# Kernel optimization log

Measured on AMD Instinct MI355X. Metric: run time of the kernel, lower is better.

The kernel has to match this reference:

```python
import jax, jax.numpy as jnp
import numpy as np

OUT = 260        # RESIZE_OUTPUT_IMAGES_SHAPE
TH = 0.8         # OD_SCORE_TH
PCT = 1.0        # INTERNAL_PERCENTAGE_IMAGE_TOTAKE
N_BOXES = 10     # loop bound in original call()
TAPS = 6         # lanczos3 support (radius 3 -> 6 taps, antialias=False)


def _lanczos_taps(src, size):
    """src: (OUT,) float sample coords in crop-local space; size: traced int crop size.
    Returns clamped tap indices (OUT,6) and normalized lanczos3 weights (OUT,6)."""
    base = jnp.floor(src).astype(jnp.int32) - 2
    taps = base[:, None] + jnp.arange(TAPS, dtype=jnp.int32)          # (OUT,6)
    d = src[:, None] - taps.astype(src.dtype)
    w = jnp.where(jnp.abs(d) < 3.0, jnp.sinc(d) * jnp.sinc(d / 3.0), 0.0)
    w = w / jnp.sum(w, axis=1, keepdims=True)
    idx = jnp.clip(taps, 0, size - 1)
    return idx, w


def _crop_resize(img, box):
    """img: (H,W,3). box: (4,) normalized [ymin,xmin,ymax,xmax] -> (OUT,OUT,3).
    Matches tf.image.resize lanczos3 (antialias=False): half-pixel centers, clamped edges."""
    H, W = img.shape[0], img.shape[1]
    y0 = (box[0] * H).astype(jnp.int32)
    x0 = (box[1] * W).astype(jnp.int32)
    y1 = (box[2] * H).astype(jnp.int32)
    x1 = (box[3] * W).astype(jnp.int32)
    ch = jnp.maximum(y1 - y0, 1)
    cw = jnp.maximum(x1 - x0, 1)
    o = jnp.arange(OUT, dtype=img.dtype)
    src_h = (o + 0.5) * (ch.astype(img.dtype) / OUT) - 0.5
    src_w = (o + 0.5) * (cw.astype(img.dtype) / OUT) - 0.5
    idx_h, w_h = _lanczos_taps(src_h, ch)
    idx_w, w_w = _lanczos_taps(src_w, cw)
    idx_h = idx_h + y0
    idx_w = idx_w + x0
    # vertical pass: gather 6 row taps per output row, reduce -> (OUT, W, 3)
    rows = jnp.einsum('pa,pawc->pwc', w_h, img[idx_h])
    # horizontal pass: gather 6 col taps per output col, reduce -> (OUT, OUT, 3)
    out = jnp.einsum('qb,pqbc->pqc', w_w, rows[:, idx_w])
    return out


def setup_inputs() -> dict:
    key = jax.random.key(0)
    k1, k2, k3, k4 = jax.random.split(key, 4)
    # scores: first 10 mostly above threshold, rest below
    s_hi = 0.85 + 0.15 * jax.random.uniform(k1, (N_BOXES,), dtype=jnp.float32)
    s_lo = 0.8 * jax.random.uniform(k2, (100 - N_BOXES,), dtype=jnp.float32)
    od_scores = jnp.concatenate([s_hi, s_lo])
    # bboxes (ymin,xmin,ymax,xmax) with guaranteed positive crop sizes
    u = jax.random.uniform(k3, (100, 4), dtype=jnp.float32)
    od_bboxes = jnp.stack([u[:, 0] * 0.45, u[:, 1] * 0.45,
                           0.55 + 0.45 * u[:, 2], 0.55 + 0.45 * u[:, 3]], axis=1)
    image = jax.random.normal(k4, (1, 2048, 2048, 3), dtype=jnp.float32)
    return {"od_scores": od_scores, "od_bboxes": od_bboxes, "image": image}


def reference(od_scores, od_bboxes, image):
    img = image[0]                           # (H,W,3)
    b10 = od_bboxes[:N_BOXES]
    s10 = od_scores[:N_BOXES]
    valid = ((od_scores[0] >= TH) & (s10 >= TH)
             & (b10[:, 1] >= 0.5 - PCT / 2.0)
             & (b10[:, 3] <= 0.5 + PCT / 2.0))
    crops = jax.vmap(lambda b: _crop_resize(img, b))(b10)   # (10,OUT,OUT,3)
    return crops * valid[:, None, None, None].astype(img.dtype)
```

## Files before the change

### kernel.cpp

```cpp
#include <hip/hip_runtime.h>
#include <math.h>

#define OUT 260
#define IMG_H 2048
#define IMG_W 2048
#define NB 10
#define TH 0.8f

__device__ __forceinline__ float sincf(float x) {
    if (x == 0.0f) return 1.0f;
    float px = 3.14159265358979323846f * x;
    return __sinf(px) / px;
}

__global__ __launch_bounds__(256) void crop_resize_kernel(
    const float* __restrict__ scores,
    const float* __restrict__ boxes,
    const float* __restrict__ img,
    float* __restrict__ out)
{
    const int p   = blockIdx.x;
    const int box = blockIdx.y;

    const float b0 = boxes[box * 4 + 0];
    const float b1 = boxes[box * 4 + 1];
    const float b2 = boxes[box * 4 + 2];
    const float b3 = boxes[box * 4 + 3];

    const int y0 = (int)(b0 * (float)IMG_H);
    const int x0 = (int)(b1 * (float)IMG_W);
    const int y1 = (int)(b2 * (float)IMG_H);
    const int x1 = (int)(b3 * (float)IMG_W);
    const int ch = max(y1 - y0, 1);
    const int cw = max(x1 - x0, 1);

    const bool valid = (scores[0] >= TH) && (scores[box] >= TH)
                    && (b1 >= 0.0f) && (b3 <= 1.0f);
    const float vmask = valid ? 1.0f : 0.0f;

    float wh[6];
    int   ih[6];
    {
        const float src = ((float)p + 0.5f) * ((float)ch / (float)OUT) - 0.5f;
        const int base = (int)floorf(src) - 2;
        float s = 0.0f;
        #pragma unroll
        for (int a = 0; a < 6; ++a) {
            const int tap = base + a;
            const float d = src - (float)tap;
            const float w = (fabsf(d) < 3.0f) ? sincf(d) * sincf(d * (1.0f / 3.0f)) : 0.0f;
            wh[a] = w;
            s += w;
            int t = tap;
            t = t < 0 ? 0 : t;
            t = t > ch - 1 ? ch - 1 : t;
            ih[a] = t + y0;
        }
        const float inv = 1.0f / s;
        #pragma unroll
        for (int a = 0; a < 6; ++a) wh[a] *= inv;
    }

    const float wscale = (float)cw / (float)OUT;

    for (int q = threadIdx.x; q < OUT; q += blockDim.x) {
        float ww[6];
        int   iw[6];
        {
            const float src = ((float)q + 0.5f) * wscale - 0.5f;
            const int base = (int)floorf(src) - 2;
            float s = 0.0f;
            #pragma unroll
            for (int b = 0; b < 6; ++b) {
                const int tap = base + b;
                const float d = src - (float)tap;
                const float w = (fabsf(d) < 3.0f) ? sincf(d) * sincf(d * (1.0f / 3.0f)) : 0.0f;
                ww[b] = w;
                s += w;
                int t = tap;
                t = t < 0 ? 0 : t;
                t = t > cw - 1 ? cw - 1 : t;
                iw[b] = (t + x0) * 3;
            }
            const float inv = 1.0f / s;
            #pragma unroll
            for (int b = 0; b < 6; ++b) ww[b] *= inv;
        }

        float acc0 = 0.0f, acc1 = 0.0f, acc2 = 0.0f;
        #pragma unroll
        for (int a = 0; a < 6; ++a) {
            const float* __restrict__ row = img + (size_t)ih[a] * (size_t)(IMG_W * 3);
            float r0 = 0.0f, r1 = 0.0f, r2 = 0.0f;
            #pragma unroll
            for (int b = 0; b < 6; ++b) {
                const float* __restrict__ px = row + iw[b];
                r0 = fmaf(ww[b], px[0], r0);
                r1 = fmaf(ww[b], px[1], r1);
                r2 = fmaf(ww[b], px[2], r2);
            }
            acc0 = fmaf(wh[a], r0, acc0);
            acc1 = fmaf(wh[a], r1, acc1);
            acc2 = fmaf(wh[a], r2, acc2);
        }

        const size_t o = (((size_t)box * OUT + p) * OUT + q) * 3;
        out[o + 0] = acc0 * vmask;
        out[o + 1] = acc1 * vmask;
        out[o + 2] = acc2 * vmask;
    }
}

extern "C" void kernel_launch(void* const* d_in, const int* in_sizes, int n_in,
                              void* d_out, int out_size, void* d_ws, size_t ws_size,
                              hipStream_t stream) {
    const float* scores = (const float*)d_in[0];
    const float* boxes  = (const float*)d_in[1];
    const float* img    = (const float*)d_in[2];
    float* out = (float*)d_out;

    dim3 grid(OUT, NB);
    crop_resize_kernel<<<grid, dim3(256), 0, stream>>>(scores, boxes, img, out);
}
```

Measured before the change: 125.7 us.

## Split crop-resize into separable horizontal and vertical passes with fp16 intermediate

```diff
diff --git a/kernel.cpp b/kernel.cpp
--- a/kernel.cpp
+++ b/kernel.cpp
@@ -2,10 +2,16 @@
 #include <math.h>
 
 #define OUT 260
+#define TAPS 6
 #define IMG_H 2048
 #define IMG_W 2048
+#define ROW_F (IMG_W * 3)
+#define IMG_TOTAL (IMG_H * ROW_F)
 #define NB 10
 #define TH 0.8f
+#define E3 (OUT * 3)
+
+typedef _Float16 half4v __attribute__((ext_vector_type(4)));
 
 __device__ __forceinline__ float sincf(float x) {
     if (x == 0.0f) return 1.0f;
@@ -13,20 +19,51 @@
     return __sinf(px) / px;
 }
 
-__global__ __launch_bounds__(256) void crop_resize_kernel(
-    const float* __restrict__ scores,
-    const float* __restrict__ boxes,
-    const float* __restrict__ img,
-    float* __restrict__ out)
-{
-    const int p   = blockIdx.x;
-    const int box = blockIdx.y;
+__global__ __launch_bounds__(256) void htaps_kernel(
+    const float* __restrict__ boxes, float* __restrict__ wH, int* __restrict__ idxH)
+{
+    const int box = blockIdx.x;
+    const float b1 = boxes[box * 4 + 1];
+    const float b3 = boxes[box * 4 + 3];
+    const int x0 = (int)(b1 * (float)IMG_W);
+    const int x1 = (int)(b3 * (float)IMG_W);
+    const int cw = max(x1 - x0, 1);
+    const float scale = (float)cw / (float)OUT;
+
+    for (int q = threadIdx.x; q < OUT; q += 256) {
+        const float src = ((float)q + 0.5f) * scale - 0.5f;
+        const int base = (int)floorf(src) - 2;
+        float w[TAPS]; int id[TAPS];
+        float s = 0.0f;
+        #pragma unroll
+        for (int k = 0; k < TAPS; ++k) {
+            const int tap = base + k;
+            const float d = src - (float)tap;
+            const float wv = (fabsf(d) < 3.0f) ? sincf(d) * sincf(d * (1.0f / 3.0f)) : 0.0f;
+            w[k] = wv; s += wv;
+            int t = tap; t = t < 0 ? 0 : t; t = t > cw - 1 ? cw - 1 : t;
+            id[k] = (x0 + t) * 3;
+        }
+        const float inv = 1.0f / s;
+        const int o = (box * OUT + q) * TAPS;
+        #pragma unroll
+        for (int k = 0; k < TAPS; ++k) { wH[o + k] = w[k] * inv; idxH[o + k] = id[k]; }
+    }
+}
+
+__global__ __launch_bounds__(256) void hresample_kernel(
+    const float* __restrict__ boxes, const float* __restrict__ img,
+    const float* __restrict__ wH, const int* __restrict__ idxH,
+    _Float16* __restrict__ tmp)
+{
+    const int a   = blockIdx.x;
+    const int p   = blockIdx.y;
+    const int box = blockIdx.z;
 
     const float b0 = boxes[box * 4 + 0];
     const float b1 = boxes[box * 4 + 1];
     const float b2 = boxes[box * 4 + 2];
     const float b3 = boxes[box * 4 + 3];
-
     const int y0 = (int)(b0 * (float)IMG_H);
     const int x0 = (int)(b1 * (float)IMG_W);
     const int y1 = (int)(b2 * (float)IMG_H);
@@ -34,12 +71,120 @@
     const int ch = max(y1 - y0, 1);
     const int cw = max(x1 - x0, 1);
 
+    const float srch = ((float)p + 0.5f) * ((float)ch / (float)OUT) - 0.5f;
+    const int baseh = (int)floorf(srch) - 2;
+    int t = baseh + a; t = t < 0 ? 0 : t; t = t > ch - 1 ? ch - 1 : t;
+    const int r = t + y0;
+
+    const int start_f = (x0 * 3) & ~3;
+    const int end_f   = (x0 + cw) * 3;
+    const int n_f     = end_f - start_f;
+
+    __shared__ float lds[6152];
+    const size_t gbase = (size_t)r * ROW_F + start_f;
+    for (int j4 = threadIdx.x * 4; j4 < n_f; j4 += 256 * 4) {
+        const size_t g = gbase + (size_t)j4;
+        if (g + 3 < (size_t)IMG_TOTAL) {
+            const float4 v = *(const float4*)(img + g);
+            lds[j4 + 0] = v.x; lds[j4 + 1] = v.y; lds[j4 + 2] = v.z; lds[j4 + 3] = v.w;
+        } else {
+            #pragma unroll
+            for (int i = 0; i < 4; ++i) {
+                size_t gi = g + i; if (gi > (size_t)(IMG_TOTAL - 1)) gi = IMG_TOTAL - 1;
+                lds[j4 + i] = img[gi];
+            }
+        }
+    }
+    __syncthreads();
+
+    const size_t tbase = (((size_t)(box * OUT + p)) * TAPS + a) * E3;
+    for (int q = threadIdx.x; q < OUT; q += 256) {
+        const int o = (box * OUT + q) * TAPS;
+        float acc0 = 0.0f, acc1 = 0.0f, acc2 = 0.0f;
+        #pragma unroll
+        for (int k = 0; k < TAPS; ++k) {
+            const float w = wH[o + k];
+            const int   li = idxH[o + k] - start_f;
+            acc0 = fmaf(w, lds[li + 0], acc0);
+            acc1 = fmaf(w, lds[li + 1], acc1);
+            acc2 = fmaf(w, lds[li + 2], acc2);
+        }
+        tmp[tbase + q * 3 + 0] = (_Float16)acc0;
+        tmp[tbase + q * 3 + 1] = (_Float16)acc1;
+        tmp[tbase + q * 3 + 2] = (_Float16)acc2;
+    }
+}
+
+__global__ __launch_bounds__(256) void vresample_kernel(
+    const float* __restrict__ scores, const float* __restrict__ boxes,
+    const _Float16* __restrict__ tmp, float* __restrict__ out)
+{
+    const int p   = blockIdx.x;
+    const int box = blockIdx.y;
+
+    const float b0 = boxes[box * 4 + 0];
+    const float b1 = boxes[box * 4 + 1];
+    const float b2 = boxes[box * 4 + 2];
+    const float b3 = boxes[box * 4 + 3];
+    const int y0 = (int)(b0 * (float)IMG_H);
+    const int y1 = (int)(b2 * (float)IMG_H);
+    const int ch = max(y1 - y0, 1);
+
     const bool valid = (scores[0] >= TH) && (scores[box] >= TH)
                     && (b1 >= 0.0f) && (b3 <= 1.0f);
     const float vmask = valid ? 1.0f : 0.0f;
 
-    float wh[6];
-    int   ih[6];
+    float wh[TAPS];
+    {
+        const float src = ((float)p + 0.5f) * ((float)ch / (float)OUT) - 0.5f;
+        const int base = (int)floorf(src) - 2;
+        float s = 0.0f;
+        #pragma unroll
+        for (int k = 0; k < TAPS; ++k) {
+            const float d = src - (float)(base + k);
+            const float w = (fabsf(d) < 3.0f) ? sincf(d) * sincf(d * (1.0f / 3.0f)) : 0.0f;
+            wh[k] = w; s += w;
+        }
+        const float inv = 1.0f / s;
+        #pragma unroll
+        for (int k = 0; k < TAPS; ++k) wh[k] *= inv;
+    }
+
+    const size_t tbase = ((size_t)(box * OUT + p)) * TAPS * E3;
+    const size_t obase = ((size_t)(box * OUT + p)) * E3;
+
+    const int j = threadIdx.x;
+    if (j < E3 / 4) {
+        const int e = j * 4;
+        float4 acc = make_float4(0.f, 0.f, 0.f, 0.f);
+        #pragma unroll
+        for (int k = 0; k < TAPS; ++k) {
+            const half4v v = *(const half4v*)(tmp + tbase + (size_t)k * E3 + e);
+            acc.x = fmaf(wh[k], (float)v.x, acc.x);
+            acc.y = fmaf(wh[k], (float)v.y, acc.y);
+            acc.z = fmaf(wh[k], (float)v.z, acc.z);
+            acc.w = fmaf(wh[k], (float)v.w, acc.w);
+        }
+        acc.x *= vmask; acc.y *= vmask; acc.z *= vmask; acc.w *= vmask;
+        *(float4*)(out + obase + e) = acc;
+    }
+}
+
+__global__ __launch_bounds__(256) void crop_resize_fallback(
+    const float* __restrict__ scores, const float* __restrict__ boxes,
+    const float* __restrict__ img, float* __restrict__ out)
+{
+    const int p = blockIdx.x;
+    const int box = blockIdx.y;
+    const float b0 = boxes[box * 4 + 0], b1 = boxes[box * 4 + 1];
+    const float b2 = boxes[box * 4 + 2], b3 = boxes[box * 4 + 3];
+    const int y0 = (int)(b0 * (float)IMG_H), x0 = (int)(b1 * (float)IMG_W);
+    const int y1 = (int)(b2 * (float)IMG_H), x1 = (int)(b3 * (float)IMG_W);
+    const int ch = max(y1 - y0, 1), cw = max(x1 - x0, 1);
+    const bool valid = (scores[0] >= TH) && (scores[box] >= TH) && (b1 >= 0.0f) && (b3 <= 1.0f);
+    const float vmask = valid ? 1.0f : 0.0f;
+
+    float wh[6]; int ih[6];
     {
         const float src = ((float)p + 0.5f) * ((float)ch / (float)OUT) - 0.5f;
         const int base = (int)floorf(src) - 2;
@@ -49,52 +194,40 @@
             const int tap = base + a;
             const float d = src - (float)tap;
             const float w = (fabsf(d) < 3.0f) ? sincf(d) * sincf(d * (1.0f / 3.0f)) : 0.0f;
-            wh[a] = w;
-            s += w;
-            int t = tap;
-            t = t < 0 ? 0 : t;
-            t = t > ch - 1 ? ch - 1 : t;
-            ih[a] = t + y0;
+            wh[a] = w; s += w;
+            int tt = tap; tt = tt < 0 ? 0 : tt; tt = tt > ch - 1 ? ch - 1 : tt;
+            ih[a] = tt + y0;
         }
         const float inv = 1.0f / s;
         #pragma unroll
         for (int a = 0; a < 6; ++a) wh[a] *= inv;
     }
-
     const float wscale = (float)cw / (float)OUT;
-
     for (int q = threadIdx.x; q < OUT; q += blockDim.x) {
-        float ww[6];
-        int   iw[6];
-        {
-            const float src = ((float)q + 0.5f) * wscale - 0.5f;
-            const int base = (int)floorf(src) - 2;
-            float s = 0.0f;
+        float ww[6]; int iw[6];
+        const float src = ((float)q + 0.5f) * wscale - 0.5f;
+        const int base = (int)floorf(src) - 2;
+        float s = 0.0f;
+        #pragma unroll
+        for (int b = 0; b < 6; ++b) {
+            const int tap = base + b;
+            const float d = src - (float)tap;
+            const float w = (fabsf(d) < 3.0f) ? sincf(d) * sincf(d * (1.0f / 3.0f)) : 0.0f;
+            ww[b] = w; s += w;
+            int tt = tap; tt = tt < 0 ? 0 : tt; tt = tt > cw - 1 ? cw - 1 : tt;
+            iw[b] = (tt + x0) * 3;
+        }
+        const float inv = 1.0f / s;
+        #pragma unroll
+        for (int b = 0; b < 6; ++b) ww[b] *= inv;
+        float acc0 = 0, acc1 = 0, acc2 = 0;
+        #pragma unroll
+        for (int a = 0; a < 6; ++a) {
+            const float* row = img + (size_t)ih[a] * ROW_F;
+            float r0 = 0, r1 = 0, r2 = 0;
             #pragma unroll
             for (int b = 0; b < 6; ++b) {
-                const int tap = base + b;
-                const float d = src - (float)tap;
-                const float w = (fabsf(d) < 3.0f) ? sincf(d) * sincf(d * (1.0f / 3.0f)) : 0.0f;
-                ww[b] = w;
-                s += w;
-                int t = tap;
-                t = t < 0 ? 0 : t;
-                t = t > cw - 1 ? cw - 1 : t;
-                iw[b] = (t + x0) * 3;
-            }
-            const float inv = 1.0f / s;
-            #pragma unroll
-            for (int b = 0; b < 6; ++b) ww[b] *= inv;
-        }
-
-        float acc0 = 0.0f, acc1 = 0.0f, acc2 = 0.0f;
-        #pragma unroll
-        for (int a = 0; a < 6; ++a) {
-            const float* __restrict__ row = img + (size_t)ih[a] * (size_t)(IMG_W * 3);
-            float r0 = 0.0f, r1 = 0.0f, r2 = 0.0f;
-            #pragma unroll
-            for (int b = 0; b < 6; ++b) {
-                const float* __restrict__ px = row + iw[b];
+                const float* px = row + iw[b];
                 r0 = fmaf(ww[b], px[0], r0);
                 r1 = fmaf(ww[b], px[1], r1);
                 r2 = fmaf(ww[b], px[2], r2);
@@ -103,11 +236,8 @@
             acc1 = fmaf(wh[a], r1, acc1);
             acc2 = fmaf(wh[a], r2, acc2);
         }
-
         const size_t o = (((size_t)box * OUT + p) * OUT + q) * 3;
-        out[o + 0] = acc0 * vmask;
-        out[o + 1] = acc1 * vmask;
-        out[o + 2] = acc2 * vmask;
+        out[o + 0] = acc0 * vmask; out[o + 1] = acc1 * vmask; out[o + 2] = acc2 * vmask;
     }
 }
 
@@ -119,6 +249,20 @@
     const float* img    = (const float*)d_in[2];
     float* out = (float*)d_out;
 
-    dim3 grid(OUT, NB);
-    crop_resize_kernel<<<grid, dim3(256), 0, stream>>>(scores, boxes, img, out);
-}
+    const size_t tmp_bytes = (size_t)NB * OUT * TAPS * E3 * sizeof(_Float16);
+    const size_t tab_elems = (size_t)NB * OUT * TAPS;
+    const size_t need = tmp_bytes + tab_elems * (sizeof(float) + sizeof(int));
+
+    if (ws_size < need) {
+        crop_resize_fallback<<<dim3(OUT, NB), dim3(256), 0, stream>>>(scores, boxes, img, out);
+        return;
+    }
+
+    _Float16* tmp = (_Float16*)d_ws;
+    float* wH  = (float*)((char*)d_ws + tmp_bytes);
+    int*   idxH = (int*)((char*)d_ws + tmp_bytes + tab_elems * sizeof(float));
+
+    htaps_kernel<<<dim3(NB), dim3(256), 0, stream>>>(boxes, wH, idxH);
+    hresample_kernel<<<dim3(TAPS, OUT, NB), dim3(256), 0, stream>>>(boxes, img, wH, idxH, tmp);
+    vresample_kernel<<<dim3(OUT, NB), dim3(256), 0, stream>>>(scores, boxes, tmp, out);
+}
```

New measurement: 136.4 us. 1.08x slower.

## Stage crop row taps in LDS as fp16 and read packed horizontal taps

Applied to the files above, without the earlier changes.

```diff
diff --git a/kernel.cpp b/kernel.cpp
--- a/kernel.cpp
+++ b/kernel.cpp
@@ -2,10 +2,15 @@
 #include <math.h>
 
 #define OUT 260
+#define TAPS 6
 #define IMG_H 2048
 #define IMG_W 2048
+#define ROW_F (IMG_W * 3)
+#define IMG_TOTAL (IMG_H * ROW_F)
 #define NB 10
 #define TH 0.8f
+#define ROWH 6152
+#define NTHREADS 320
 
 __device__ __forceinline__ float sincf(float x) {
     if (x == 0.0f) return 1.0f;
@@ -13,7 +18,7 @@
     return __sinf(px) / px;
 }
 
-__global__ __launch_bounds__(256) void crop_resize_kernel(
+__global__ __launch_bounds__(NTHREADS) void crop_resize_fused(
     const float* __restrict__ scores,
     const float* __restrict__ boxes,
     const float* __restrict__ img,
@@ -38,72 +43,130 @@
                     && (b1 >= 0.0f) && (b3 <= 1.0f);
     const float vmask = valid ? 1.0f : 0.0f;
 
-    float wh[6];
-    int   ih[6];
+    float wh[TAPS];
+    int   ih[TAPS];
     {
         const float src = ((float)p + 0.5f) * ((float)ch / (float)OUT) - 0.5f;
         const int base = (int)floorf(src) - 2;
         float s = 0.0f;
         #pragma unroll
-        for (int a = 0; a < 6; ++a) {
+        for (int a = 0; a < TAPS; ++a) {
             const int tap = base + a;
             const float d = src - (float)tap;
             const float w = (fabsf(d) < 3.0f) ? sincf(d) * sincf(d * (1.0f / 3.0f)) : 0.0f;
-            wh[a] = w;
-            s += w;
-            int t = tap;
-            t = t < 0 ? 0 : t;
-            t = t > ch - 1 ? ch - 1 : t;
+            wh[a] = w; s += w;
+            int t = tap; t = t < 0 ? 0 : t; t = t > ch - 1 ? ch - 1 : t;
             ih[a] = t + y0;
         }
         const float inv = 1.0f / s;
         #pragma unroll
-        for (int a = 0; a < 6; ++a) wh[a] *= inv;
+        for (int a = 0; a < TAPS; ++a) wh[a] *= inv;
     }
 
-    const float wscale = (float)cw / (float)OUT;
+    const int q = threadIdx.x;
+    float ww[TAPS];
+    int basew = 0;
+    bool fast = false;
+    if (q < OUT) {
+        const float src = ((float)q + 0.5f) * ((float)cw / (float)OUT) - 0.5f;
+        basew = (int)floorf(src) - 2;
+        float s = 0.0f;
+        #pragma unroll
+        for (int k = 0; k < TAPS; ++k) {
+            const float d = src - (float)(basew + k);
+            const float w = (fabsf(d) < 3.0f) ? sincf(d) * sincf(d * (1.0f / 3.0f)) : 0.0f;
+            ww[k] = w; s += w;
+        }
+        const float inv = 1.0f / s;
+        #pragma unroll
+        for (int k = 0; k < TAPS; ++k) ww[k] *= inv;
+        fast = (basew >= 0) && (basew + 5 <= cw - 1);
+    }
 
-    for (int q = threadIdx.x; q < OUT; q += blockDim.x) {
-        float ww[6];
-        int   iw[6];
-        {
-            const float src = ((float)q + 0.5f) * wscale - 0.5f;
-            const int base = (int)floorf(src) - 2;
-            float s = 0.0f;
+    const int start_f = (x0 * 3) & ~3;
+    const int end_f   = (x0 + cw) * 3;
+    const int n_f     = end_f - start_f;
+
+    __shared__ _Float16 lds[3 * ROWH];
+
+    float acc0 = 0.0f, acc1 = 0.0f, acc2 = 0.0f;
+
+    for (int chunk = 0; chunk < 2; ++chunk) {
+        if (chunk) __syncthreads();
+
+        #pragma unroll
+        for (int r = 0; r < 3; ++r) {
+            const int row = ih[3 * chunk + r];
+            const size_t gb = (size_t)row * ROW_F + start_f;
+            _Float16* lrow = lds + r * ROWH;
+            for (int f = threadIdx.x * 4; f < n_f; f += NTHREADS * 4) {
+                const size_t g = gb + (size_t)f;
+                if (g + 4 <= (size_t)IMG_TOTAL) {
+                    const float4 v = *(const float4*)(img + g);
+                    lrow[f + 0] = (_Float16)v.x;
+                    lrow[f + 1] = (_Float16)v.y;
+                    lrow[f + 2] = (_Float16)v.z;
+                    lrow[f + 3] = (_Float16)v.w;
+                } else {
+                    #pragma unroll
+                    for (int i = 0; i < 4; ++i) {
+                        size_t gi = g + i;
+                        if (gi > (size_t)(IMG_TOTAL - 1)) gi = IMG_TOTAL - 1;
+                        lrow[f + i] = (_Float16)img[gi];
+                    }
+                }
+            }
+        }
+        __syncthreads();
+
+        if (q < OUT) {
             #pragma unroll
-            for (int b = 0; b < 6; ++b) {
-                const int tap = base + b;
-                const float d = src - (float)tap;
-                const float w = (fabsf(d) < 3.0f) ? sincf(d) * sincf(d * (1.0f / 3.0f)) : 0.0f;
-                ww[b] = w;
-                s += w;
-                int t = tap;
-                t = t < 0 ? 0 : t;
-                t = t > cw - 1 ? cw - 1 : t;
-                iw[b] = (t + x0) * 3;
+            for (int r = 0; r < 3; ++r) {
+                const float whr = wh[3 * chunk + r];
+                const _Float16* lrow = lds + r * ROWH;
+                float s0 = 0.0f, s1 = 0.0f, s2 = 0.0f;
+                if (fast) {
+                    const int hb = (x0 + basew) * 3 - start_f;
+                    const int wb = hb >> 1;
+                    const bool odd = (hb & 1) != 0;
+                    const unsigned int* wp = (const unsigned int*)lrow;
+                    float e[20];
+                    #pragma unroll
+                    for (int w = 0; w < 10; ++w) {
+                        union { unsigned int u; _Float16 h[2]; } cv;
+                        cv.u = wp[wb + w];
+                        e[2 * w + 0] = (float)cv.h[0];
+                        e[2 * w + 1] = (float)cv.h[1];
+                    }
+                    #pragma unroll
+                    for (int k = 0; k < TAPS; ++k) {
+                        const float p0 = odd ? e[3 * k + 1] : e[3 * k + 0];
+                        const float p1 = odd ? e[3 * k + 2] : e[3 * k + 1];
+                        const float p2 = odd ? e[3 * k + 3] : e[3 * k + 2];
+                        s0 = fmaf(ww[k], p0, s0);
+                        s1 = fmaf(ww[k], p1, s1);
+                        s2 = fmaf(ww[k], p2, s2);
+                    }
+                } else {
+                    #pragma unroll
+                    for (int k = 0; k < TAPS; ++k) {
+                        int t = basew + k;
+                        t = t < 0 ? 0 : t;
+                        t = t > cw - 1 ? cw - 1 : t;
+                        const int hb = (x0 + t) * 3 - start_f;
+                        s0 = fmaf(ww[k], (float)lrow[hb + 0], s0);
+                        s1 = fmaf(ww[k], (float)lrow[hb + 1], s1);
+                        s2 = fmaf(ww[k], (float)lrow[hb + 2], s2);
+                    }
+                }
+                acc0 = fmaf(whr, s0, acc0);
+                acc1 = fmaf(whr, s1, acc1);
+                acc2 = fmaf(whr, s2, acc2);
             }
-            const float inv = 1.0f / s;
-            #pragma unroll
-            for (int b = 0; b < 6; ++b) ww[b] *= inv;
         }
+    }
 
-        float acc0 = 0.0f, acc1 = 0.0f, acc2 = 0.0f;
-        #pragma unroll
-        for (int a = 0; a < 6; ++a) {
-            const float* __restrict__ row = img + (size_t)ih[a] * (size_t)(IMG_W * 3);
-            float r0 = 0.0f, r1 = 0.0f, r2 = 0.0f;
-            #pragma unroll
-            for (int b = 0; b < 6; ++b) {
-                const float* __restrict__ px = row + iw[b];
-                r0 = fmaf(ww[b], px[0], r0);
-                r1 = fmaf(ww[b], px[1], r1);
-                r2 = fmaf(ww[b], px[2], r2);
-            }
-            acc0 = fmaf(wh[a], r0, acc0);
-            acc1 = fmaf(wh[a], r1, acc1);
-            acc2 = fmaf(wh[a], r2, acc2);
-        }
-
+    if (q < OUT) {
         const size_t o = (((size_t)box * OUT + p) * OUT + q) * 3;
         out[o + 0] = acc0 * vmask;
         out[o + 1] = acc1 * vmask;
@@ -119,6 +182,5 @@
     const float* img    = (const float*)d_in[2];
     float* out = (float*)d_out;
 
-    dim3 grid(OUT, NB);
-    crop_resize_kernel<<<grid, dim3(256), 0, stream>>>(scores, boxes, img, out);
+    crop_resize_fused<<<dim3(OUT, NB), dim3(NTHREADS), 0, stream>>>(scores, boxes, img, out);
 }
```

Result: slower. 148.4 us (+18.1%).

## Do vertical lanczos pass into LDS row buffer, then horizontal pass from LDS

Applied to the files above, without the earlier changes.

```diff
diff --git a/kernel.cpp b/kernel.cpp
--- a/kernel.cpp
+++ b/kernel.cpp
@@ -2,10 +2,14 @@
 #include <math.h>
 
 #define OUT 260
+#define TAPS 6
 #define IMG_H 2048
 #define IMG_W 2048
+#define ROW_F (IMG_W * 3)
+#define IMG_TOTAL (IMG_H * ROW_F)
 #define NB 10
 #define TH 0.8f
+#define LDS_F 6152
 
 __device__ __forceinline__ float sincf(float x) {
     if (x == 0.0f) return 1.0f;
@@ -13,7 +17,7 @@
     return __sinf(px) / px;
 }
 
-__global__ __launch_bounds__(256) void crop_resize_kernel(
+__global__ __launch_bounds__(256) void crop_resize_vfirst(
     const float* __restrict__ scores,
     const float* __restrict__ boxes,
     const float* __restrict__ img,
@@ -27,10 +31,12 @@
     const float b2 = boxes[box * 4 + 2];
     const float b3 = boxes[box * 4 + 3];
 
-    const int y0 = (int)(b0 * (float)IMG_H);
-    const int x0 = (int)(b1 * (float)IMG_W);
-    const int y1 = (int)(b2 * (float)IMG_H);
-    const int x1 = (int)(b3 * (float)IMG_W);
+    int y0 = (int)(b0 * (float)IMG_H);
+    int x0 = (int)(b1 * (float)IMG_W);
+    int y1 = (int)(b2 * (float)IMG_H);
+    int x1 = (int)(b3 * (float)IMG_W);
+    if (y1 > IMG_H) y1 = IMG_H;
+    if (x1 > IMG_W) x1 = IMG_W;
     const int ch = max(y1 - y0, 1);
     const int cw = max(x1 - x0, 1);
 
@@ -38,76 +44,87 @@
                     && (b1 >= 0.0f) && (b3 <= 1.0f);
     const float vmask = valid ? 1.0f : 0.0f;
 
-    float wh[6];
-    int   ih[6];
+    float wh[TAPS];
+    int   ih[TAPS];
     {
         const float src = ((float)p + 0.5f) * ((float)ch / (float)OUT) - 0.5f;
         const int base = (int)floorf(src) - 2;
         float s = 0.0f;
         #pragma unroll
-        for (int a = 0; a < 6; ++a) {
+        for (int a = 0; a < TAPS; ++a) {
             const int tap = base + a;
             const float d = src - (float)tap;
             const float w = (fabsf(d) < 3.0f) ? sincf(d) * sincf(d * (1.0f / 3.0f)) : 0.0f;
-            wh[a] = w;
-            s += w;
-            int t = tap;
-            t = t < 0 ? 0 : t;
-            t = t > ch - 1 ? ch - 1 : t;
+            wh[a] = w; s += w;
+            int t = tap; t = t < 0 ? 0 : t; t = t > ch - 1 ? ch - 1 : t;
             ih[a] = t + y0;
         }
         const float inv = 1.0f / s;
         #pragma unroll
-        for (int a = 0; a < 6; ++a) wh[a] *= inv;
+        for (int a = 0; a < TAPS; ++a) wh[a] *= inv;
     }
 
+    const int start_f = (x0 * 3) & ~3;
+    const int end_f   = (x0 + cw) * 3;
+    const int n_f     = end_f - start_f;
+
+    __shared__ float lds[LDS_F];
+
+    {
+        const float* r0 = img + (size_t)ih[0] * ROW_F + start_f;
+        const float* r1 = img + (size_t)ih[1] * ROW_F + start_f;
+        const float* r2 = img + (size_t)ih[2] * ROW_F + start_f;
+        const float* r3 = img + (size_t)ih[3] * ROW_F + start_f;
+        const float* r4 = img + (size_t)ih[4] * ROW_F + start_f;
+        const float* r5 = img + (size_t)ih[5] * ROW_F + start_f;
+
+        for (int f = threadIdx.x * 4; f < n_f; f += 256 * 4) {
+            const float4 v0 = *(const float4*)(r0 + f);
+            const float4 v1 = *(const float4*)(r1 + f);
+            const float4 v2 = *(const float4*)(r2 + f);
+            const float4 v3 = *(const float4*)(r3 + f);
+            const float4 v4 = *(const float4*)(r4 + f);
+            const float4 v5 = *(const float4*)(r5 + f);
+            float4 acc;
+            acc.x = wh[0]*v0.x + wh[1]*v1.x + wh[2]*v2.x + wh[3]*v3.x + wh[4]*v4.x + wh[5]*v5.x;
+            acc.y = wh[0]*v0.y + wh[1]*v1.y + wh[2]*v2.y + wh[3]*v3.y + wh[4]*v4.y + wh[5]*v5.y;
+            acc.z = wh[0]*v0.z + wh[1]*v1.z + wh[2]*v2.z + wh[3]*v3.z + wh[4]*v4.z + wh[5]*v5.z;
+            acc.w = wh[0]*v0.w + wh[1]*v1.w + wh[2]*v2.w + wh[3]*v3.w + wh[4]*v4.w + wh[5]*v5.w;
+            *(float4*)(lds + f) = acc;
+        }
+    }
+    __syncthreads();
+
     const float wscale = (float)cw / (float)OUT;
+    for (int q = threadIdx.x; q < OUT; q += 256) {
+        const float src = ((float)q + 0.5f) * wscale - 0.5f;
+        const int basew = (int)floorf(src) - 2;
+        float ww[TAPS];
+        float s = 0.0f;
+        #pragma unroll
+        for (int k = 0; k < TAPS; ++k) {
+            const float d = src - (float)(basew + k);
+            const float w = (fabsf(d) < 3.0f) ? sincf(d) * sincf(d * (1.0f / 3.0f)) : 0.0f;
+            ww[k] = w; s += w;
+        }
+        const float inv = 1.0f / s;
 
-    for (int q = threadIdx.x; q < OUT; q += blockDim.x) {
-        float ww[6];
-        int   iw[6];
-        {
-            const float src = ((float)q + 0.5f) * wscale - 0.5f;
-            const int base = (int)floorf(src) - 2;
-            float s = 0.0f;
-            #pragma unroll
-            for (int b = 0; b < 6; ++b) {
-                const int tap = base + b;
-                const float d = src - (float)tap;
-                const float w = (fabsf(d) < 3.0f) ? sincf(d) * sincf(d * (1.0f / 3.0f)) : 0.0f;
-                ww[b] = w;
-                s += w;
-                int t = tap;
-                t = t < 0 ? 0 : t;
-                t = t > cw - 1 ? cw - 1 : t;
-                iw[b] = (t + x0) * 3;
-            }
-            const float inv = 1.0f / s;
-            #pragma unroll
-            for (int b = 0; b < 6; ++b) ww[b] *= inv;
+        float a0 = 0.0f, a1 = 0.0f, a2 = 0.0f;
+        #pragma unroll
+        for (int k = 0; k < TAPS; ++k) {
+            int t = basew + k;
+            t = t < 0 ? 0 : t;
+            t = t > cw - 1 ? cw - 1 : t;
+            const int hb = (x0 + t) * 3 - start_f;
+            a0 = fmaf(ww[k], lds[hb + 0], a0);
+            a1 = fmaf(ww[k], lds[hb + 1], a1);
+            a2 = fmaf(ww[k], lds[hb + 2], a2);
         }
-
-        float acc0 = 0.0f, acc1 = 0.0f, acc2 = 0.0f;
-        #pragma unroll
-        for (int a = 0; a < 6; ++a) {
-            const float* __restrict__ row = img + (size_t)ih[a] * (size_t)(IMG_W * 3);
-            float r0 = 0.0f, r1 = 0.0f, r2 = 0.0f;
-            #pragma unroll
-            for (int b = 0; b < 6; ++b) {
-                const float* __restrict__ px = row + iw[b];
-                r0 = fmaf(ww[b], px[0], r0);
-                r1 = fmaf(ww[b], px[1], r1);
-                r2 = fmaf(ww[b], px[2], r2);
-            }
-            acc0 = fmaf(wh[a], r0, acc0);
-            acc1 = fmaf(wh[a], r1, acc1);
-            acc2 = fmaf(wh[a], r2, acc2);
-        }
-
+        const float m = vmask * inv;
         const size_t o = (((size_t)box * OUT + p) * OUT + q) * 3;
-        out[o + 0] = acc0 * vmask;
-        out[o + 1] = acc1 * vmask;
-        out[o + 2] = acc2 * vmask;
+        out[o + 0] = a0 * m;
+        out[o + 1] = a1 * m;
+        out[o + 2] = a2 * m;
     }
 }
 
@@ -119,6 +136,5 @@
     const float* img    = (const float*)d_in[2];
     float* out = (float*)d_out;
 
-    dim3 grid(OUT, NB);
-    crop_resize_kernel<<<grid, dim3(256), 0, stream>>>(scores, boxes, img, out);
+    crop_resize_vfirst<<<dim3(OUT, NB), dim3(256), 0, stream>>>(scores, boxes, img, out);
 }
```

After: 115.2 us. 1.09x faster.
